# Kernel tuning notes

Measured on AMD Instinct MI355X. Metric: run time of the kernel, lower is better.

Reference implementation:

```python
import jax, jax.numpy as jnp
import numpy as np

STRIDES = (8, 16, 32, 64, 128)
NUM_CLASSES = 80
TOPK = 1000
CONF_THRESH = 0.05
NMS_THRESH = 0.6
IMG_H = IMG_W = 2048
CLASS_OFFSET = 100000.0  # > any box coordinate, makes different-class boxes disjoint


def _level_decode(cls, reg, ctn, scale, stride):
    # cls: [1,C,H,W], reg: [1,4,H,W], ctn: [1,1,H,W]
    C, H, W = cls.shape[1], cls.shape[2], cls.shape[3]
    cls = jnp.transpose(cls[0], (1, 2, 0)).reshape(-1, C)       # [HW, C]
    reg = jnp.transpose(reg[0], (1, 2, 0)).reshape(-1, 4)       # [HW, 4]
    reg = jax.nn.relu(reg * scale) * stride                      # Scale + relu + stride
    ctn = jnp.transpose(ctn[0], (1, 2, 0)).reshape(-1, 1)       # [HW, 1]
    prob = jnp.sqrt(jax.nn.sigmoid(cls) * jax.nn.sigmoid(ctn))  # [HW, C]
    scores = prob.max(axis=-1)
    labels = prob.argmax(axis=-1)
    ys, xs = jnp.meshgrid(jnp.arange(H), jnp.arange(W), indexing='ij')
    anchors = (jnp.stack([xs, ys], axis=-1).reshape(-1, 2).astype(cls.dtype) + 0.5) * stride
    if scores.shape[0] > TOPK:
        scores, idx = jax.lax.top_k(scores, TOPK)
        labels, reg, anchors = labels[idx], reg[idx], anchors[idx]
    # decode (l,t,r,b) deltas around anchor centers -> (x1,y1,x2,y2)
    boxes = jnp.concatenate([anchors - reg[:, :2], anchors + reg[:, 2:]], axis=-1)
    return scores, labels, boxes


def _nms_keep(boxes, scores, valid, thresh):
    # Sequential greedy NMS, same math as the numpy loop in RTEFCOS.nms.
    order = jnp.argsort(-jnp.where(valid, scores, -jnp.inf))
    b = boxes[order]
    v = valid[order]
    x1, y1, x2, y2 = b[:, 0], b[:, 1], b[:, 2], b[:, 3]
    areas = (x2 - x1) * (y2 - y1)
    n = b.shape[0]
    pos = jnp.arange(n)

    def body(i, keep):
        xx1 = jnp.maximum(x1[i], x1)
        yy1 = jnp.maximum(y1[i], y1)
        xx2 = jnp.minimum(x2[i], x2)
        yy2 = jnp.minimum(y2[i], y2)
        inter = jnp.maximum(1e-10, xx2 - xx1) * jnp.maximum(1e-10, yy2 - yy1)
        ovr = inter / (areas[i] + areas - inter + 1e-14)
        suppress = (ovr > thresh) & (pos > i) & keep[i]
        return keep & (~suppress)

    keep_sorted = jax.lax.fori_loop(0, n, body, v)
    return jnp.zeros(n, dtype=bool).at[order].set(keep_sorted)


def reference(cls0, reg0, ctn0, cls1, reg1, ctn1, cls2, reg2, ctn2,
              cls3, reg3, ctn3, cls4, reg4, ctn4, scales):
    levels = [(cls0, reg0, ctn0), (cls1, reg1, ctn1), (cls2, reg2, ctn2),
              (cls3, reg3, ctn3), (cls4, reg4, ctn4)]
    all_s, all_l, all_b = [], [], []
    for lv, (c, r, t) in enumerate(levels):
        s, l, b = _level_decode(c, r, t, scales[lv], STRIDES[lv])
        all_s.append(s); all_l.append(l); all_b.append(b)
    scores = jnp.concatenate(all_s)   # [M]
    labels = jnp.concatenate(all_l)   # [M]
    bboxes = jnp.concatenate(all_b)   # [M, 4]
    valid = scores >= CONF_THRESH     # conf filter as mask (static shapes)
    # class-wise NMS via coordinate-offset trick: boxes of different classes
    # never overlap, so one greedy pass == per-class greedy passes.
    boxes_off = bboxes + labels[:, None].astype(bboxes.dtype) * CLASS_OFFSET
    keep = _nms_keep(boxes_off, scores, valid, NMS_THRESH)
    bboxes = bboxes / jnp.array([IMG_W, IMG_H, IMG_W, IMG_H], dtype=bboxes.dtype)
    bboxes = jnp.clip(bboxes, 0.0, 1.0)
    return bboxes, scores, labels, keep


def setup_inputs():
    key = jax.random.key(0)
    ks = jax.random.split(key, len(STRIDES))
    inp = {}
    for lv, stride in enumerate(STRIDES):
        H = IMG_H // stride
        W = IMG_W // stride
        k1, k2, k3 = jax.random.split(ks[lv], 3)
        inp[f"cls{lv}"] = jax.random.normal(k1, (1, NUM_CLASSES, H, W), jnp.float32)
        inp[f"reg{lv}"] = jax.random.uniform(k2, (1, 4, H, W), jnp.float32)
        inp[f"ctn{lv}"] = jax.random.normal(k3, (1, 1, H, W), jnp.float32)
    inp["scales"] = jnp.ones((5,), jnp.float32)
    return inp
```

## Files before the change

### kernel.cpp

```cpp
#include <hip/hip_runtime.h>
#include <math.h>

#define TOTAL_ANCHORS 87296
#define NTOPK 87040
#define NSEL 4256
#define NWORDS 67
#define NPAD   4288
#define MAXROUNDS 4300
#define CANDMAX 8192
#define NBIN 32768
#define NSLAB 8

__device__ __forceinline__ float sigmoidf_(float x) {
    return 1.0f / (1.0f + expf(-x));
}
__device__ __forceinline__ unsigned int f2s(float f) {
    unsigned int u = __float_as_uint(f);
    return u ^ ((u >> 31) ? 0xFFFFFFFFu : 0x80000000u);
}
__device__ __forceinline__ float s2f(unsigned int k) {
    unsigned int u = (k & 0x80000000u) ? (k ^ 0x80000000u) : ~k;
    return __uint_as_float(u);
}
__device__ __forceinline__ void level_of(int g, int& lv, int& base, int& W, int& stride) {
    if (g < 65536)      { lv = 0; base = 0;     W = 256; stride = 8;   }
    else if (g < 81920) { lv = 1; base = 65536; W = 128; stride = 16;  }
    else if (g < 86016) { lv = 2; base = 81920; W = 64;  stride = 32;  }
    else if (g < 87040) { lv = 3; base = 86016; W = 32;  stride = 64;  }
    else                { lv = 4; base = 87040; W = 16;  stride = 128; }
}

struct InPtrs {
    const float* cls[5];
    const float* reg[5];
    const float* ctn[5];
    const float* scales;
};

__global__ __launch_bounds__(256) void cmax_kernel(InPtrs in,
        unsigned long long* __restrict__ cmax2) {
    int a = blockIdx.x * 256 + threadIdx.x;
    int cg = blockIdx.y;
    int lv, base, W, stride;
    level_of(a, lv, base, W, stride);
    (void)stride;
    int p = a - base;
    int HW = W * W;
    const float* cls = in.cls[lv];
    float sctn = sigmoidf_(in.ctn[lv][p]);
    int c0 = cg * 8;
    float v[8];
    #pragma unroll
    for (int k = 0; k < 8; ++k) v[k] = cls[(c0 + k) * HW + p];
    unsigned long long best = 0ull;
    #pragma unroll
    for (int k = 0; k < 8; ++k) {
        float pr = sqrtf(__fmul_rn(sigmoidf_(v[k]), sctn));
        unsigned long long key = ((unsigned long long)f2s(pr) << 32)
                               | (unsigned long long)(255 - (c0 + k));
        best = (key > best) ? key : best;
    }
    cmax2[(size_t)cg * TOTAL_ANCHORS + a] = best;
}

__global__ __launch_bounds__(256) void decode2_kernel(InPtrs in,
        const unsigned long long* __restrict__ cmax2,
        unsigned long long* __restrict__ keys, float* __restrict__ scores,
        int* __restrict__ labels, float4* __restrict__ boxes) {
    int g = blockIdx.x * 256 + threadIdx.x;
    int lv, base, W, stride;
    level_of(g, lv, base, W, stride);
    int p = g - base;
    int HW = W * W;
    int x = p & (W - 1);
    int y = p / W;
    unsigned long long mk = 0ull;
    #pragma unroll
    for (int cg = 0; cg < 10; ++cg) {
        unsigned long long v = cmax2[(size_t)cg * TOTAL_ANCHORS + g];
        mk = (v > mk) ? v : mk;
    }
    float best = s2f((unsigned int)(mk >> 32));
    int lbl = 255 - (int)(mk & 0xFFull);
    float scale = in.scales[lv];
    float fs = (float)stride;
    const float* rg = in.reg[lv];
    float r0 = __fmul_rn(fmaxf(__fmul_rn(rg[0 * HW + p], scale), 0.0f), fs);
    float r1 = __fmul_rn(fmaxf(__fmul_rn(rg[1 * HW + p], scale), 0.0f), fs);
    float r2 = __fmul_rn(fmaxf(__fmul_rn(rg[2 * HW + p], scale), 0.0f), fs);
    float r3 = __fmul_rn(fmaxf(__fmul_rn(rg[3 * HW + p], scale), 0.0f), fs);
    float ax = __fmul_rn(__fadd_rn((float)x, 0.5f), fs);
    float ay = __fmul_rn(__fadd_rn((float)y, 0.5f), fs);
    float4 b;
    b.x = __fsub_rn(ax, r0);
    b.y = __fsub_rn(ay, r1);
    b.z = __fadd_rn(ax, r2);
    b.w = __fadd_rn(ay, r3);
    scores[g] = best;
    labels[g] = lbl;
    boxes[g]  = b;
    keys[g] = (mk & 0xFFFFFFFF00000000ull)
            | (unsigned long long)(unsigned int)(~(unsigned int)p);
}

__global__ __launch_bounds__(1024) void hist_kernel(
        const unsigned long long* __restrict__ keys,
        unsigned int* __restrict__ slab) {
    __shared__ unsigned int h[NBIN / 2];
    const int starts[NSLAB] = {0, 16384, 32768, 49152, 65536, 73728, 81920, 86016};
    const int ends[NSLAB]   = {16384, 32768, 49152, 65536, 73728, 81920, 86016, 87040};
    const int tid = threadIdx.x;
    for (int i = tid; i < NBIN / 2; i += 1024) h[i] = 0u;
    __syncthreads();
    const int s = starts[blockIdx.x], e = ends[blockIdx.x];
    for (int i = s + tid; i < e; i += 1024) {
        unsigned int bin = (unsigned int)(keys[i] >> 48) & 0x7FFFu;
        atomicAdd(&h[bin >> 1], 1u << ((bin & 1u) << 4));
    }
    __syncthreads();
    unsigned int* out = slab + blockIdx.x * (NBIN / 2);
    for (int i = tid; i < NBIN / 2; i += 1024) out[i] = h[i];
}

__global__ __launch_bounds__(1024) void select_kernel(
        const unsigned int* __restrict__ slab, unsigned int* __restrict__ thr,
        unsigned int* __restrict__ cnt) {
    const int lvl = blockIdx.x;
    const int slabS[4] = {0, 4, 6, 7};
    const int slabE[4] = {4, 6, 7, 8};
    const int tid = threadIdx.x;
    if (lvl == 0 && tid < 128) cnt[tid] = 0u;
    __shared__ unsigned int csum[1024];
    unsigned int s = 0;
    for (int sb = slabS[lvl]; sb < slabE[lvl]; ++sb) {
        const unsigned int* A = slab + sb * (NBIN / 2);
        #pragma unroll 4
        for (int w = tid * 16; w < tid * 16 + 16; ++w) {
            unsigned int v = A[w];
            s += (v & 0xFFFFu) + (v >> 16);
        }
    }
    csum[tid] = s;
    __syncthreads();
    for (int off = 1; off < 1024; off <<= 1) {
        unsigned int v = csum[tid] + ((tid + off < 1024) ? csum[tid + off] : 0u);
        __syncthreads();
        csum[tid] = v;
        __syncthreads();
    }
    unsigned int incl = csum[tid];
    unsigned int incl1 = (tid == 1023) ? 0u : csum[tid + 1];
    if (incl >= 1000u && incl1 < 1000u) {
        unsigned int running = incl1;
        for (int b = tid * 32 + 31; b >= tid * 32; --b) {
            unsigned int c = 0;
            for (int sb = slabS[lvl]; sb < slabE[lvl]; ++sb) {
                unsigned int v = slab[sb * (NBIN / 2) + (b >> 1)];
                c += (v >> ((b & 1) << 4)) & 0xFFFFu;
            }
            running += c;
            if (running >= 1000u) { thr[lvl] = (unsigned int)b; break; }
        }
    }
}

__global__ __launch_bounds__(1024) void gather_kernel(
        const unsigned long long* __restrict__ keys,
        const unsigned int* __restrict__ thr,
        unsigned long long* __restrict__ cand, unsigned int* __restrict__ cnt) {
    int g = blockIdx.x * 1024 + threadIdx.x;
    int lvl;
    if (g < 65536)      lvl = 0;
    else if (g < 81920) lvl = 1;
    else if (g < 86016) lvl = 2;
    else                lvl = 3;
    unsigned long long k = keys[g];
    bool pass = (((unsigned int)(k >> 48)) & 0x7FFFu) >= thr[lvl];
    __shared__ unsigned int woff[16];
    __shared__ unsigned int base_;
    const int wave = threadIdx.x >> 6, lane = threadIdx.x & 63;
    unsigned long long m = __ballot(pass);
    if (lane == 0) woff[wave] = (unsigned int)__popcll(m);
    __syncthreads();
    if (threadIdx.x == 0) {
        unsigned int tot = 0;
        #pragma unroll
        for (int w = 0; w < 16; ++w) { unsigned int c = woff[w]; woff[w] = tot; tot += c; }
        base_ = atomicAdd(&cnt[lvl << 5], tot);
    }
    __syncthreads();
    if (pass) {
        unsigned int pos = base_ + woff[wave]
                         + (unsigned int)__popcll(m & ((1ull << lane) - 1ull));
        if (pos < CANDMAX) cand[(lvl << 13) + pos] = k;
    }
}

__global__ __launch_bounds__(1024) void finalsort_kernel(
        const unsigned long long* __restrict__ cand,
        const unsigned int* __restrict__ cnt,
        unsigned long long* __restrict__ sel) {
    const int lvl = blockIdx.x;
    const int tid = threadIdx.x;
    __shared__ unsigned long long sk[CANDMAX];
    int n = (int)cnt[lvl << 5];
    if (n > CANDMAX) n = CANDMAX;
    int P = 1024;
    while (P < n) P <<= 1;
    for (int i = tid; i < P; i += 1024)
        sk[i] = (i < n) ? cand[(lvl << 13) + i] : 0ull;
    __syncthreads();
    for (int kk = 2; kk <= P; kk <<= 1) {
        for (int j = kk >> 1; j > 0; j >>= 1) {
            for (int i = tid; i < P; i += 1024) {
                int ixj = i ^ j;
                if (ixj > i) {
                    unsigned long long a = sk[i], b = sk[ixj];
                    bool sw = ((i & kk) == 0) ? (a < b) : (a > b);
                    if (sw) { sk[i] = b; sk[ixj] = a; }
                }
            }
            __syncthreads();
        }
    }
    if (tid < 1000) sel[lvl * 1000 + tid] = sk[tid];
}

#define PEND_VEC 3216
__global__ __launch_bounds__(256) void fin_kernel(
        const unsigned long long* __restrict__ sel,
        const float* __restrict__ scores, const int* __restrict__ labels,
        const float4* __restrict__ boxes, float* __restrict__ out,
        float4* __restrict__ entbox, float* __restrict__ entarea,
        int* __restrict__ entvalid, unsigned long long* __restrict__ ekeyG,
        float4* __restrict__ pendzero) {
    int pos = blockIdx.x * 256 + threadIdx.x;
    if (pos < PEND_VEC) pendzero[pos] = make_float4(0.f, 0.f, 0.f, 0.f);
    if (pos >= NSEL) return;
    int g;
    if (pos < 4000) {
        int lv = pos / 1000;
        const int offs_[4] = {0, 65536, 81920, 86016};
        unsigned long long key = sel[pos];
        unsigned int p = ~((unsigned int)(key & 0xFFFFFFFFull));
        g = offs_[lv] + (int)p;
    } else {
        g = 87040 + (pos - 4000);
    }
    float sc = scores[g];
    int lb = labels[g];
    float4 bx = boxes[g];
    const float inv = 1.0f / 2048.0f;
    out[pos * 4 + 0] = fminf(fmaxf(__fmul_rn(bx.x, inv), 0.0f), 1.0f);
    out[pos * 4 + 1] = fminf(fmaxf(__fmul_rn(bx.y, inv), 0.0f), 1.0f);
    out[pos * 4 + 2] = fminf(fmaxf(__fmul_rn(bx.z, inv), 0.0f), 1.0f);
    out[pos * 4 + 3] = fminf(fmaxf(__fmul_rn(bx.w, inv), 0.0f), 1.0f);
    out[17024 + pos] = sc;
    out[21280 + pos] = (float)lb;
    out[25536 + pos] = 0.0f;
    float off = __fmul_rn((float)lb, 100000.0f);
    float4 eb;
    eb.x = __fadd_rn(bx.x, off); eb.y = __fadd_rn(bx.y, off);
    eb.z = __fadd_rn(bx.z, off); eb.w = __fadd_rn(bx.w, off);
    entbox[pos] = eb;
    entarea[pos] = __fmul_rn(__fsub_rn(eb.z, eb.x), __fsub_rn(eb.w, eb.y));
    int valid = (sc >= 0.05f) ? 1 : 0;
    entvalid[pos] = valid;
    float effs = valid ? sc : -INFINITY;
    ekeyG[pos] = ((unsigned long long)f2s(effs) << 32) | (unsigned int)(~(unsigned int)pos);
}

__device__ __forceinline__ int count_greater(const unsigned long long* A, int n,
                                             unsigned long long x) {
    int lo = 0, hi = n;
    while (lo < hi) { int m = (lo + hi) >> 1; if (A[m] > x) lo = m + 1; else hi = m; }
    return lo;
}
__global__ __launch_bounds__(1024) void rank_kernel(
        const unsigned long long* __restrict__ ekeyG,
        const float4* __restrict__ entbox, const float* __restrict__ entarea,
        const int* __restrict__ entvalid,
        int* __restrict__ order, float4* __restrict__ sbox,
        float* __restrict__ sarea, int* __restrict__ svalid) {
    __shared__ unsigned long long eL[4000];
    __shared__ unsigned long long sk4[256];
    const int tid = threadIdx.x;
    for (int i = tid; i < 4000; i += 1024) eL[i] = ekeyG[i];
    if (tid < 256) sk4[tid] = ekeyG[4000 + tid];
    __syncthreads();
    for (int kk = 2; kk <= 256; kk <<= 1) {
        for (int j = kk >> 1; j > 0; j >>= 1) {
            if (tid < 256) {
                int ixj = tid ^ j;
                if (ixj > tid) {
                    unsigned long long a = sk4[tid], b = sk4[ixj];
                    bool sw = ((tid & kk) == 0) ? (a < b) : (a > b);
                    if (sw) { sk4[tid] = b; sk4[ixj] = a; }
                }
            }
            __syncthreads();
        }
    }
    int pos = blockIdx.x * 1024 + tid;
    if (pos < NSEL) {
        unsigned long long x = (pos < 4000) ? eL[pos] : ekeyG[pos];
        int rank = count_greater(eL,        1000, x)
                 + count_greater(eL + 1000, 1000, x)
                 + count_greater(eL + 2000, 1000, x)
                 + count_greater(eL + 3000, 1000, x)
                 + count_greater(sk4,        256, x);
        order[rank]  = pos;
        sbox[rank]   = entbox[pos];
        sarea[rank]  = entarea[pos];
        svalid[rank] = entvalid[pos];
    }
}

__global__ __launch_bounds__(64) void mask_kernel(
        const float4* __restrict__ sbox, const float* __restrict__ sarea,
        const int* __restrict__ svalid,
        unsigned long long* __restrict__ maskC,
        unsigned long long* __restrict__ pend0G,
        unsigned int* __restrict__ pend1G) {
    int colTile = blockIdx.x, rowTile = blockIdx.y;
    if (colTile > rowTile) return;
    __shared__ float4 cb[64];
    __shared__ float ca[64];
    int tid = threadIdx.x;
    int col0 = colTile * 64;
    int c = col0 + tid;
    int vcol = 0;
    if (c < NSEL) { cb[tid] = sbox[c]; ca[tid] = sarea[c]; vcol = svalid[c]; }
    else { cb[tid] = make_float4(0.f, 0.f, 0.f, 0.f); ca[tid] = 0.f; }
    unsigned long long unkw = __ballot(vcol != 0);
    __syncthreads();
    int i = rowTile * 64 + tid;
    unsigned long long bits = 0ull;
    if (i < NSEL) {
        float4 b = sbox[i];
        float ar = sarea[i];
        for (int j = 0; j < 64; ++j) {
            float xx1 = fmaxf(b.x, cb[j].x);
            float yy1 = fmaxf(b.y, cb[j].y);
            float xx2 = fminf(b.z, cb[j].z);
            float yy2 = fminf(b.w, cb[j].w);
            float w = fmaxf(1e-10f, __fsub_rn(xx2, xx1));
            float h = fmaxf(1e-10f, __fsub_rn(yy2, yy1));
            float inter = __fmul_rn(w, h);
            float denom = __fadd_rn(__fsub_rn(__fadd_rn(ar, ca[j]), inter), 1e-14f);
            float ovr = __fdiv_rn(inter, denom);
            if (ovr > 0.6f) bits |= (1ull << j);
        }
    }
    maskC[(size_t)colTile * NPAD + i] = bits;
    if (colTile < rowTile && i < NSEL && (bits & unkw)) {
        if (colTile < 64) atomicOr(&pend0G[i], 1ull << colTile);
        else              atomicOr(&pend1G[i], 1u << (colTile - 64));
    }
}

__global__ __launch_bounds__(1024) void sweep_kernel(
        const unsigned long long* __restrict__ maskC,
        const unsigned long long* __restrict__ pend0G,
        const unsigned int* __restrict__ pend1G,
        const int* __restrict__ order, const int* __restrict__ svalid,
        float* __restrict__ out_keep) {
    const int tid = threadIdx.x;
    const int lane = tid & 63;
    const int wave = tid >> 6;
    __shared__ unsigned long long keptL[NWORDS], unkL[NWORDS];
    __shared__ unsigned long long nk[NWORDS], nkC[NWORDS], ndC[NWORDS];
    __shared__ unsigned long long cm0s;
    __shared__ unsigned int cm1s;
    __shared__ int anych;
    __shared__ int wflag[16];

    unsigned long long md[5], pend0[5];
    unsigned int pendH[5];
    #pragma unroll
    for (int k = 0; k < 5; ++k) {
        int b = wave + 16 * k;
        unsigned long long w = 0ull;
        md[k] = 0ull; pend0[k] = 0ull; pendH[k] = 0u;
        if (b < NWORDS) {
            int c = b * 64 + lane;
            int v = (c < NSEL) ? svalid[c] : 0;
            w = __ballot(v != 0);
            md[k]    = maskC[(size_t)b * NPAD + c];
            pend0[k] = pend0G[c];
            pendH[k] = pend1G[c];
            if (lane == 0) { unkL[b] = w; keptL[b] = 0ull; nk[b] = 0ull; }
        }
    }
    if (tid == 0) { cm0s = 0ull; cm1s = 0u; }
    __syncthreads();

    for (int round = 0; round < MAXROUNDS; ++round) {
        unsigned long long cm0 = cm0s;
        unsigned int cm1 = cm1s;
        #pragma unroll
        for (int k = 0; k < 5; ++k) {
            int b = wave + 16 * k;
            bool kp = false, dec = false;
            if (b < NWORDS) {
                int c = b * 64 + lane;
                unsigned long long uw = unkL[b];
                if ((uw >> lane) & 1ull) {
                    bool rem = false;
                    unsigned long long todo = pend0[k] & cm0;
                    while (todo) {
                        int w = __ffsll((long long)todo) - 1;
                        todo &= todo - 1ull;
                        unsigned long long m = maskC[(size_t)w * NPAD + c];
                        if (m & nk[w]) { rem = true; break; }
                        if ((m & unkL[w]) == 0ull) pend0[k] &= ~(1ull << w);
                    }
                    if (!rem) {
                        unsigned int todoH = pendH[k] & cm1;
                        while (todoH) {
                            int bit = __ffs(todoH) - 1;
                            todoH &= todoH - 1u;
                            int w = 64 + bit;
                            unsigned long long m = maskC[(size_t)w * NPAD + c];
                            if (m & nk[w]) { rem = true; break; }
                            if ((m & unkL[w]) == 0ull) pendH[k] &= ~(1u << bit);
                        }
                    }
                    unsigned long long below = (1ull << lane) - 1ull;
                    if (!rem && (md[k] & keptL[b] & below)) rem = true;
                    if (!rem && pend0[k] == 0ull && pendH[k] == 0u
                             && (md[k] & uw & below) == 0ull) kp = true;
                    dec = rem || kp;
                }
            }
            unsigned long long kb = __ballot(kp);
            unsigned long long db = __ballot(dec);
            if (b < NWORDS && lane == 0) { nkC[b] = kb; ndC[b] = db; }
        }
        __syncthreads();
        int any = 0;
        #pragma unroll
        for (int k = 0; k < 5; ++k) {
            int b = wave + 16 * k;
            if (b >= NWORDS) continue;
            unsigned long long db = ndC[b];
            if (lane == 0) {
                keptL[b] |= nkC[b];
                unkL[b]  &= ~db;
                nk[b]     = nkC[b];
            }
            any |= (db != 0ull) ? 1 : 0;
        }
        if (lane == 0) wflag[wave] = any;
        __syncthreads();
        if (tid == 0) {
            unsigned long long c0 = 0ull; unsigned int c1 = 0u; int a = 0;
            for (int w = 0; w < 64; ++w) if (ndC[w]) c0 |= (1ull << w);
            for (int w = 64; w < NWORDS; ++w) if (ndC[w]) c1 |= (1u << (w - 64));
            #pragma unroll
            for (int w = 0; w < 16; ++w) a |= wflag[w];
            cm0s = c0; cm1s = c1; anych = a;
        }
        __syncthreads();
        if (!anych) break;
    }

    #pragma unroll
    for (int k = 0; k < 5; ++k) {
        int b = wave + 16 * k;
        if (b >= NWORDS) continue;
        int c = b * 64 + lane;
        if (c < NSEL && ((keptL[b] >> lane) & 1ull)) out_keep[order[c]] = 1.0f;
    }
}

constexpr size_t OFF_KEYS    = 0;
constexpr size_t OFF_SCORES  = OFF_KEYS    + 698368;
constexpr size_t OFF_LABELS  = OFF_SCORES  + 349184;
constexpr size_t OFF_BOXES   = OFF_LABELS  + 349184;
constexpr size_t OFF_SEL     = OFF_BOXES   + 1396736;
constexpr size_t OFF_ORDER   = OFF_SEL     + 32000;
constexpr size_t OFF_SBOX    = OFF_ORDER   + 17024;
constexpr size_t OFF_SAREA   = OFF_SBOX    + 68096;
constexpr size_t OFF_SVALID  = OFF_SAREA   + 17024;
constexpr size_t OFF_MASK    = OFF_SVALID  + 17024;
constexpr size_t OFF_CMAX2   = OFF_MASK    + (size_t)NWORDS * NPAD * 8;
constexpr size_t OFF_CNT     = OFF_CMAX2   + 10u * 698368u;
constexpr size_t OFF_PEND0   = OFF_CNT     + 512;
constexpr size_t OFF_PEND1   = OFF_PEND0   + (size_t)NPAD * 8;
constexpr size_t OFF_THR     = OFF_PEND1   + (size_t)NPAD * 4;
constexpr size_t OFF_SLAB    = OFF_THR     + 64;
constexpr size_t OFF_CAND    = OFF_SLAB    + (size_t)NSLAB * 16384u * 4u;
constexpr size_t OFF_EKEY    = OFF_CAND    + 4u * CANDMAX * 8u;
constexpr size_t OFF_ENTBOX  = OFF_EKEY    + 34048;
constexpr size_t OFF_ENTAREA = OFF_ENTBOX  + 68096;
constexpr size_t OFF_ENTVAL  = OFF_ENTAREA + 17024;

extern "C" void kernel_launch(void* const* d_in, const int* in_sizes, int n_in,
                              void* d_out, int out_size, void* d_ws, size_t ws_size,
                              hipStream_t stream) {
    (void)in_sizes; (void)n_in; (void)out_size; (void)ws_size;
    InPtrs P;
    for (int lv = 0; lv < 5; ++lv) {
        P.cls[lv] = (const float*)d_in[3 * lv + 0];
        P.reg[lv] = (const float*)d_in[3 * lv + 1];
        P.ctn[lv] = (const float*)d_in[3 * lv + 2];
    }
    P.scales = (const float*)d_in[15];

    char* ws = (char*)d_ws;
    unsigned long long* keys   = (unsigned long long*)(ws + OFF_KEYS);
    float*              scores = (float*)             (ws + OFF_SCORES);
    int*                labels = (int*)               (ws + OFF_LABELS);
    float4*             boxes  = (float4*)            (ws + OFF_BOXES);
    unsigned long long* sel    = (unsigned long long*)(ws + OFF_SEL);
    int*                order  = (int*)               (ws + OFF_ORDER);
    float4*             sbox   = (float4*)            (ws + OFF_SBOX);
    float*              sarea  = (float*)             (ws + OFF_SAREA);
    int*                svalid = (int*)               (ws + OFF_SVALID);
    unsigned long long* maskb  = (unsigned long long*)(ws + OFF_MASK);
    unsigned long long* cmax2  = (unsigned long long*)(ws + OFF_CMAX2);
    unsigned int*       cnt    = (unsigned int*)      (ws + OFF_CNT);
    unsigned long long* pend0  = (unsigned long long*)(ws + OFF_PEND0);
    unsigned int*       pend1  = (unsigned int*)      (ws + OFF_PEND1);
    unsigned int*       thr    = (unsigned int*)      (ws + OFF_THR);
    unsigned int*       slab   = (unsigned int*)      (ws + OFF_SLAB);
    unsigned long long* cand   = (unsigned long long*)(ws + OFF_CAND);
    unsigned long long* ekeyG  = (unsigned long long*)(ws + OFF_EKEY);
    float4*             entbox = (float4*)            (ws + OFF_ENTBOX);
    float*              entarea= (float*)             (ws + OFF_ENTAREA);
    int*                entval = (int*)               (ws + OFF_ENTVAL);
    float* out = (float*)d_out;

    cmax_kernel<<<dim3(341, 10), 256, 0, stream>>>(P, cmax2);
    decode2_kernel<<<341, 256, 0, stream>>>(P, cmax2, keys, scores, labels, boxes);
    hist_kernel<<<NSLAB, 1024, 0, stream>>>(keys, slab);
    select_kernel<<<4, 1024, 0, stream>>>(slab, thr, cnt);
    gather_kernel<<<85, 1024, 0, stream>>>(keys, thr, cand, cnt);
    finalsort_kernel<<<4, 1024, 0, stream>>>(cand, cnt, sel);
    fin_kernel<<<(NSEL + 255) / 256, 256, 0, stream>>>(sel, scores, labels, boxes, out,
                                                       entbox, entarea, entval, ekeyG,
                                                       (float4*)(ws + OFF_PEND0));
    rank_kernel<<<(NSEL + 1023) / 1024, 1024, 0, stream>>>(ekeyG, entbox, entarea, entval,
                                                           order, sbox, sarea, svalid);
    mask_kernel<<<dim3(NWORDS, NWORDS), 64, 0, stream>>>(sbox, sarea, svalid,
                                                         maskb, pend0, pend1);
    sweep_kernel<<<1, 1024, 0, stream>>>(maskb, pend0, pend1, order, svalid, out + 25536);
}
```

Measured before the change: 120.8 us.

## Vectorize decode kernels, fuse fin into rank, batch mask rows per block

The cmax and decode kernels now handle four anchors per thread with float4 and 128-bit loads and stores. The fin kernel is merged into the rank kernel, so each block rebuilds the sort keys in shared memory and writes the outputs and sorted boxes directly, which removes one launch and the intermediate global buffers. Zeroing of the pending buffers moves into the gather kernel. The mask kernel processes four row tiles per 256-thread block so each column tile is loaded once for all four, at the cost of every finrank block recomputing all keys.

```diff
diff --git a/kernel.cpp b/kernel.cpp
--- a/kernel.cpp
+++ b/kernel.cpp
@@ -10,6 +10,7 @@
 #define CANDMAX 8192
 #define NBIN 32768
 #define NSLAB 8
+#define PEND_VEC 3216
 
 __device__ __forceinline__ float sigmoidf_(float x) {
     return 1.0f / (1.0f + expf(-x));
@@ -21,6 +22,9 @@
 __device__ __forceinline__ float s2f(unsigned int k) {
     unsigned int u = (k & 0x80000000u) ? (k ^ 0x80000000u) : ~k;
     return __uint_as_float(u);
+}
+__device__ __forceinline__ float f4e(const float4& v, int j) {
+    return (j == 0) ? v.x : ((j == 1) ? v.y : ((j == 2) ? v.z : v.w));
 }
 __device__ __forceinline__ void level_of(int g, int& lv, int& base, int& W, int& stride) {
     if (g < 65536)      { lv = 0; base = 0;     W = 256; stride = 8;   }
@@ -39,68 +43,97 @@
 
 __global__ __launch_bounds__(256) void cmax_kernel(InPtrs in,
         unsigned long long* __restrict__ cmax2) {
-    int a = blockIdx.x * 256 + threadIdx.x;
+    int t = blockIdx.x * 256 + threadIdx.x;
+    int a0 = t * 4;
+    if (a0 >= TOTAL_ANCHORS) return;
     int cg = blockIdx.y;
     int lv, base, W, stride;
-    level_of(a, lv, base, W, stride);
+    level_of(a0, lv, base, W, stride);
     (void)stride;
-    int p = a - base;
+    int p0 = a0 - base;
     int HW = W * W;
     const float* cls = in.cls[lv];
-    float sctn = sigmoidf_(in.ctn[lv][p]);
+    float4 ct = *(const float4*)&in.ctn[lv][p0];
+    float sct0 = sigmoidf_(ct.x), sct1 = sigmoidf_(ct.y);
+    float sct2 = sigmoidf_(ct.z), sct3 = sigmoidf_(ct.w);
     int c0 = cg * 8;
-    float v[8];
-    #pragma unroll
-    for (int k = 0; k < 8; ++k) v[k] = cls[(c0 + k) * HW + p];
-    unsigned long long best = 0ull;
+    unsigned long long b0 = 0ull, b1 = 0ull, b2 = 0ull, b3 = 0ull;
     #pragma unroll
     for (int k = 0; k < 8; ++k) {
-        float pr = sqrtf(__fmul_rn(sigmoidf_(v[k]), sctn));
-        unsigned long long key = ((unsigned long long)f2s(pr) << 32)
-                               | (unsigned long long)(255 - (c0 + k));
-        best = (key > best) ? key : best;
-    }
-    cmax2[(size_t)cg * TOTAL_ANCHORS + a] = best;
+        float4 v = *(const float4*)&cls[(c0 + k) * HW + p0];
+        unsigned long long lbl = (unsigned long long)(255 - (c0 + k));
+        unsigned long long k0 = ((unsigned long long)f2s(sqrtf(__fmul_rn(sigmoidf_(v.x), sct0))) << 32) | lbl;
+        unsigned long long k1 = ((unsigned long long)f2s(sqrtf(__fmul_rn(sigmoidf_(v.y), sct1))) << 32) | lbl;
+        unsigned long long k2 = ((unsigned long long)f2s(sqrtf(__fmul_rn(sigmoidf_(v.z), sct2))) << 32) | lbl;
+        unsigned long long k3 = ((unsigned long long)f2s(sqrtf(__fmul_rn(sigmoidf_(v.w), sct3))) << 32) | lbl;
+        b0 = (k0 > b0) ? k0 : b0;
+        b1 = (k1 > b1) ? k1 : b1;
+        b2 = (k2 > b2) ? k2 : b2;
+        b3 = (k3 > b3) ? k3 : b3;
+    }
+    unsigned long long* dst = cmax2 + (size_t)cg * TOTAL_ANCHORS + a0;
+    dst[0] = b0; dst[1] = b1; dst[2] = b2; dst[3] = b3;
 }
 
 __global__ __launch_bounds__(256) void decode2_kernel(InPtrs in,
         const unsigned long long* __restrict__ cmax2,
         unsigned long long* __restrict__ keys, float* __restrict__ scores,
         int* __restrict__ labels, float4* __restrict__ boxes) {
-    int g = blockIdx.x * 256 + threadIdx.x;
+    int t = blockIdx.x * 256 + threadIdx.x;
+    int g0 = t * 4;
+    if (g0 >= TOTAL_ANCHORS) return;
     int lv, base, W, stride;
-    level_of(g, lv, base, W, stride);
-    int p = g - base;
+    level_of(g0, lv, base, W, stride);
+    int p0 = g0 - base;
     int HW = W * W;
-    int x = p & (W - 1);
-    int y = p / W;
-    unsigned long long mk = 0ull;
+    unsigned long long mk0 = 0ull, mk1 = 0ull, mk2 = 0ull, mk3 = 0ull;
     #pragma unroll
     for (int cg = 0; cg < 10; ++cg) {
-        unsigned long long v = cmax2[(size_t)cg * TOTAL_ANCHORS + g];
-        mk = (v > mk) ? v : mk;
-    }
-    float best = s2f((unsigned int)(mk >> 32));
-    int lbl = 255 - (int)(mk & 0xFFull);
+        const ulonglong2* s2 = (const ulonglong2*)(cmax2 + (size_t)cg * TOTAL_ANCHORS + g0);
+        ulonglong2 va = s2[0], vb = s2[1];
+        mk0 = (va.x > mk0) ? va.x : mk0;
+        mk1 = (va.y > mk1) ? va.y : mk1;
+        mk2 = (vb.x > mk2) ? vb.x : mk2;
+        mk3 = (vb.y > mk3) ? vb.y : mk3;
+    }
+    unsigned long long mk[4] = {mk0, mk1, mk2, mk3};
     float scale = in.scales[lv];
     float fs = (float)stride;
     const float* rg = in.reg[lv];
-    float r0 = __fmul_rn(fmaxf(__fmul_rn(rg[0 * HW + p], scale), 0.0f), fs);
-    float r1 = __fmul_rn(fmaxf(__fmul_rn(rg[1 * HW + p], scale), 0.0f), fs);
-    float r2 = __fmul_rn(fmaxf(__fmul_rn(rg[2 * HW + p], scale), 0.0f), fs);
-    float r3 = __fmul_rn(fmaxf(__fmul_rn(rg[3 * HW + p], scale), 0.0f), fs);
-    float ax = __fmul_rn(__fadd_rn((float)x, 0.5f), fs);
-    float ay = __fmul_rn(__fadd_rn((float)y, 0.5f), fs);
-    float4 b;
-    b.x = __fsub_rn(ax, r0);
-    b.y = __fsub_rn(ay, r1);
-    b.z = __fadd_rn(ax, r2);
-    b.w = __fadd_rn(ay, r3);
-    scores[g] = best;
-    labels[g] = lbl;
-    boxes[g]  = b;
-    keys[g] = (mk & 0xFFFFFFFF00000000ull)
-            | (unsigned long long)(unsigned int)(~(unsigned int)p);
+    float4 rq0 = *(const float4*)&rg[0 * HW + p0];
+    float4 rq1 = *(const float4*)&rg[1 * HW + p0];
+    float4 rq2 = *(const float4*)&rg[2 * HW + p0];
+    float4 rq3 = *(const float4*)&rg[3 * HW + p0];
+    float4 sc4;
+    int4 lb4;
+    #pragma unroll
+    for (int j = 0; j < 4; ++j) {
+        int p = p0 + j;
+        int x = p & (W - 1);
+        int y = p / W;
+        float best = s2f((unsigned int)(mk[j] >> 32));
+        int lbl = 255 - (int)(mk[j] & 0xFFull);
+        float r0 = __fmul_rn(fmaxf(__fmul_rn(f4e(rq0, j), scale), 0.0f), fs);
+        float r1 = __fmul_rn(fmaxf(__fmul_rn(f4e(rq1, j), scale), 0.0f), fs);
+        float r2 = __fmul_rn(fmaxf(__fmul_rn(f4e(rq2, j), scale), 0.0f), fs);
+        float r3 = __fmul_rn(fmaxf(__fmul_rn(f4e(rq3, j), scale), 0.0f), fs);
+        float ax = __fmul_rn(__fadd_rn((float)x, 0.5f), fs);
+        float ay = __fmul_rn(__fadd_rn((float)y, 0.5f), fs);
+        float4 b;
+        b.x = __fsub_rn(ax, r0);
+        b.y = __fsub_rn(ay, r1);
+        b.z = __fadd_rn(ax, r2);
+        b.w = __fadd_rn(ay, r3);
+        boxes[g0 + j] = b;
+        keys[g0 + j] = (mk[j] & 0xFFFFFFFF00000000ull)
+                     | (unsigned long long)(unsigned int)(~(unsigned int)(p));
+        if (j == 0) { sc4.x = best; lb4.x = lbl; }
+        else if (j == 1) { sc4.y = best; lb4.y = lbl; }
+        else if (j == 2) { sc4.z = best; lb4.z = lbl; }
+        else { sc4.w = best; lb4.w = lbl; }
+    }
+    *(float4*)&scores[g0] = sc4;
+    *(int4*)&labels[g0] = lb4;
 }
 
 __global__ __launch_bounds__(1024) void hist_kernel(
@@ -167,7 +200,12 @@
 __global__ __launch_bounds__(1024) void gather_kernel(
         const unsigned long long* __restrict__ keys,
         const unsigned int* __restrict__ thr,
-        unsigned long long* __restrict__ cand, unsigned int* __restrict__ cnt) {
+        unsigned long long* __restrict__ cand, unsigned int* __restrict__ cnt,
+        float4* __restrict__ pendzero) {
+    if (blockIdx.x < 4) {
+        int z = blockIdx.x * 1024 + threadIdx.x;
+        if (z < PEND_VEC) pendzero[z] = make_float4(0.f, 0.f, 0.f, 0.f);
+    }
     int g = blockIdx.x * 1024 + threadIdx.x;
     int lvl;
     if (g < 65536)      lvl = 0;
@@ -226,67 +264,46 @@
     if (tid < 1000) sel[lvl * 1000 + tid] = sk[tid];
 }
 
-#define PEND_VEC 3216
-__global__ __launch_bounds__(256) void fin_kernel(
-        const unsigned long long* __restrict__ sel,
-        const float* __restrict__ scores, const int* __restrict__ labels,
-        const float4* __restrict__ boxes, float* __restrict__ out,
-        float4* __restrict__ entbox, float* __restrict__ entarea,
-        int* __restrict__ entvalid, unsigned long long* __restrict__ ekeyG,
-        float4* __restrict__ pendzero) {
-    int pos = blockIdx.x * 256 + threadIdx.x;
-    if (pos < PEND_VEC) pendzero[pos] = make_float4(0.f, 0.f, 0.f, 0.f);
-    if (pos >= NSEL) return;
-    int g;
-    if (pos < 4000) {
-        int lv = pos / 1000;
-        const int offs_[4] = {0, 65536, 81920, 86016};
-        unsigned long long key = sel[pos];
-        unsigned int p = ~((unsigned int)(key & 0xFFFFFFFFull));
-        g = offs_[lv] + (int)p;
-    } else {
-        g = 87040 + (pos - 4000);
-    }
-    float sc = scores[g];
-    int lb = labels[g];
-    float4 bx = boxes[g];
-    const float inv = 1.0f / 2048.0f;
-    out[pos * 4 + 0] = fminf(fmaxf(__fmul_rn(bx.x, inv), 0.0f), 1.0f);
-    out[pos * 4 + 1] = fminf(fmaxf(__fmul_rn(bx.y, inv), 0.0f), 1.0f);
-    out[pos * 4 + 2] = fminf(fmaxf(__fmul_rn(bx.z, inv), 0.0f), 1.0f);
-    out[pos * 4 + 3] = fminf(fmaxf(__fmul_rn(bx.w, inv), 0.0f), 1.0f);
-    out[17024 + pos] = sc;
-    out[21280 + pos] = (float)lb;
-    out[25536 + pos] = 0.0f;
-    float off = __fmul_rn((float)lb, 100000.0f);
-    float4 eb;
-    eb.x = __fadd_rn(bx.x, off); eb.y = __fadd_rn(bx.y, off);
-    eb.z = __fadd_rn(bx.z, off); eb.w = __fadd_rn(bx.w, off);
-    entbox[pos] = eb;
-    entarea[pos] = __fmul_rn(__fsub_rn(eb.z, eb.x), __fsub_rn(eb.w, eb.y));
-    int valid = (sc >= 0.05f) ? 1 : 0;
-    entvalid[pos] = valid;
-    float effs = valid ? sc : -INFINITY;
-    ekeyG[pos] = ((unsigned long long)f2s(effs) << 32) | (unsigned int)(~(unsigned int)pos);
-}
-
 __device__ __forceinline__ int count_greater(const unsigned long long* A, int n,
                                              unsigned long long x) {
     int lo = 0, hi = n;
     while (lo < hi) { int m = (lo + hi) >> 1; if (A[m] > x) lo = m + 1; else hi = m; }
     return lo;
 }
-__global__ __launch_bounds__(1024) void rank_kernel(
-        const unsigned long long* __restrict__ ekeyG,
-        const float4* __restrict__ entbox, const float* __restrict__ entarea,
-        const int* __restrict__ entvalid,
+__global__ __launch_bounds__(1024) void finrank_kernel(
+        const unsigned long long* __restrict__ sel,
+        const float* __restrict__ scores, const int* __restrict__ labels,
+        const float4* __restrict__ boxes, float* __restrict__ out,
         int* __restrict__ order, float4* __restrict__ sbox,
         float* __restrict__ sarea, int* __restrict__ svalid) {
-    __shared__ unsigned long long eL[4000];
+    __shared__ unsigned long long eL[NSEL];
     __shared__ unsigned long long sk4[256];
     const int tid = threadIdx.x;
-    for (int i = tid; i < 4000; i += 1024) eL[i] = ekeyG[i];
-    if (tid < 256) sk4[tid] = ekeyG[4000 + tid];
+    const int blk = blockIdx.x;
+    int gown = 0; float scown = 0.f; int vown = 0;
+    #pragma unroll
+    for (int k = 0; k < 5; ++k) {
+        int pos = tid + k * 1024;
+        if (pos < NSEL) {
+            int g;
+            if (pos < 4000) {
+                int lvp = pos / 1000;
+                const int offs_[4] = {0, 65536, 81920, 86016};
+                unsigned long long key = sel[pos];
+                unsigned int p = ~((unsigned int)(key & 0xFFFFFFFFull));
+                g = offs_[lvp] + (int)p;
+            } else {
+                g = 87040 + (pos - 4000);
+            }
+            float sc = scores[g];
+            int valid = (sc >= 0.05f) ? 1 : 0;
+            float effs = valid ? sc : -INFINITY;
+            eL[pos] = ((unsigned long long)f2s(effs) << 32) | (unsigned int)(~(unsigned int)pos);
+            if (k == blk) { gown = g; scown = sc; vown = valid; }
+        }
+    }
+    __syncthreads();
+    if (tid < 256) sk4[tid] = eL[4000 + tid];
     __syncthreads();
     for (int kk = 2; kk <= 256; kk <<= 1) {
         for (int j = kk >> 1; j > 0; j >>= 1) {
@@ -301,40 +318,62 @@
             __syncthreads();
         }
     }
-    int pos = blockIdx.x * 1024 + tid;
+    int pos = blk * 1024 + tid;
     if (pos < NSEL) {
-        unsigned long long x = (pos < 4000) ? eL[pos] : ekeyG[pos];
+        int lb = labels[gown];
+        float4 bx = boxes[gown];
+        const float inv = 1.0f / 2048.0f;
+        float4 o4;
+        o4.x = fminf(fmaxf(__fmul_rn(bx.x, inv), 0.0f), 1.0f);
+        o4.y = fminf(fmaxf(__fmul_rn(bx.y, inv), 0.0f), 1.0f);
+        o4.z = fminf(fmaxf(__fmul_rn(bx.z, inv), 0.0f), 1.0f);
+        o4.w = fminf(fmaxf(__fmul_rn(bx.w, inv), 0.0f), 1.0f);
+        *(float4*)&out[pos * 4] = o4;
+        out[17024 + pos] = scown;
+        out[21280 + pos] = (float)lb;
+        out[25536 + pos] = 0.0f;
+        float off = __fmul_rn((float)lb, 100000.0f);
+        float4 eb;
+        eb.x = __fadd_rn(bx.x, off); eb.y = __fadd_rn(bx.y, off);
+        eb.z = __fadd_rn(bx.z, off); eb.w = __fadd_rn(bx.w, off);
+        float area = __fmul_rn(__fsub_rn(eb.z, eb.x), __fsub_rn(eb.w, eb.y));
+        unsigned long long x = eL[pos];
         int rank = count_greater(eL,        1000, x)
                  + count_greater(eL + 1000, 1000, x)
                  + count_greater(eL + 2000, 1000, x)
                  + count_greater(eL + 3000, 1000, x)
                  + count_greater(sk4,        256, x);
         order[rank]  = pos;
-        sbox[rank]   = entbox[pos];
-        sarea[rank]  = entarea[pos];
-        svalid[rank] = entvalid[pos];
-    }
-}
-
-__global__ __launch_bounds__(64) void mask_kernel(
+        sbox[rank]   = eb;
+        sarea[rank]  = area;
+        svalid[rank] = vown;
+    }
+}
+
+__global__ __launch_bounds__(256) void mask_kernel(
         const float4* __restrict__ sbox, const float* __restrict__ sarea,
         const int* __restrict__ svalid,
         unsigned long long* __restrict__ maskC,
         unsigned long long* __restrict__ pend0G,
         unsigned int* __restrict__ pend1G) {
-    int colTile = blockIdx.x, rowTile = blockIdx.y;
-    if (colTile > rowTile) return;
+    const int colTile = blockIdx.x;
+    const int tid = threadIdx.x;
+    const int lane = tid & 63;
+    const int rowTile = blockIdx.y * 4 + (tid >> 6);
     __shared__ float4 cb[64];
     __shared__ float ca[64];
-    int tid = threadIdx.x;
     int col0 = colTile * 64;
-    int c = col0 + tid;
-    int vcol = 0;
-    if (c < NSEL) { cb[tid] = sbox[c]; ca[tid] = sarea[c]; vcol = svalid[c]; }
-    else { cb[tid] = make_float4(0.f, 0.f, 0.f, 0.f); ca[tid] = 0.f; }
+    if (tid < 64) {
+        int c = col0 + tid;
+        if (c < NSEL) { cb[tid] = sbox[c]; ca[tid] = sarea[c]; }
+        else { cb[tid] = make_float4(0.f, 0.f, 0.f, 0.f); ca[tid] = 0.f; }
+    }
+    __syncthreads();
+    if (rowTile >= NWORDS || colTile > rowTile) return;
+    int cc = col0 + lane;
+    int vcol = (cc < NSEL) ? svalid[cc] : 0;
     unsigned long long unkw = __ballot(vcol != 0);
-    __syncthreads();
-    int i = rowTile * 64 + tid;
+    int i = rowTile * 64 + lane;
     unsigned long long bits = 0ull;
     if (i < NSEL) {
         float4 b = sbox[i];
@@ -491,10 +530,6 @@
 constexpr size_t OFF_THR     = OFF_PEND1   + (size_t)NPAD * 4;
 constexpr size_t OFF_SLAB    = OFF_THR     + 64;
 constexpr size_t OFF_CAND    = OFF_SLAB    + (size_t)NSLAB * 16384u * 4u;
-constexpr size_t OFF_EKEY    = OFF_CAND    + 4u * CANDMAX * 8u;
-constexpr size_t OFF_ENTBOX  = OFF_EKEY    + 34048;
-constexpr size_t OFF_ENTAREA = OFF_ENTBOX  + 68096;
-constexpr size_t OFF_ENTVAL  = OFF_ENTAREA + 17024;
 
 extern "C" void kernel_launch(void* const* d_in, const int* in_sizes, int n_in,
                               void* d_out, int out_size, void* d_ws, size_t ws_size,
@@ -526,24 +561,19 @@
     unsigned int*       thr    = (unsigned int*)      (ws + OFF_THR);
     unsigned int*       slab   = (unsigned int*)      (ws + OFF_SLAB);
     unsigned long long* cand   = (unsigned long long*)(ws + OFF_CAND);
-    unsigned long long* ekeyG  = (unsigned long long*)(ws + OFF_EKEY);
-    float4*             entbox = (float4*)            (ws + OFF_ENTBOX);
-    float*              entarea= (float*)             (ws + OFF_ENTAREA);
-    int*                entval = (int*)               (ws + OFF_ENTVAL);
     float* out = (float*)d_out;
 
-    cmax_kernel<<<dim3(341, 10), 256, 0, stream>>>(P, cmax2);
-    decode2_kernel<<<341, 256, 0, stream>>>(P, cmax2, keys, scores, labels, boxes);
+    const int quarter_blocks = (TOTAL_ANCHORS / 4 + 255) / 256;
+    cmax_kernel<<<dim3(quarter_blocks, 10), 256, 0, stream>>>(P, cmax2);
+    decode2_kernel<<<quarter_blocks, 256, 0, stream>>>(P, cmax2, keys, scores, labels, boxes);
     hist_kernel<<<NSLAB, 1024, 0, stream>>>(keys, slab);
     select_kernel<<<4, 1024, 0, stream>>>(slab, thr, cnt);
-    gather_kernel<<<85, 1024, 0, stream>>>(keys, thr, cand, cnt);
+    gather_kernel<<<85, 1024, 0, stream>>>(keys, thr, cand, cnt,
+                                           (float4*)(ws + OFF_PEND0));
     finalsort_kernel<<<4, 1024, 0, stream>>>(cand, cnt, sel);
-    fin_kernel<<<(NSEL + 255) / 256, 256, 0, stream>>>(sel, scores, labels, boxes, out,
-                                                       entbox, entarea, entval, ekeyG,
-                                                       (float4*)(ws + OFF_PEND0));
-    rank_kernel<<<(NSEL + 1023) / 1024, 1024, 0, stream>>>(ekeyG, entbox, entarea, entval,
-                                                           order, sbox, sarea, svalid);
-    mask_kernel<<<dim3(NWORDS, NWORDS), 64, 0, stream>>>(sbox, sarea, svalid,
-                                                         maskb, pend0, pend1);
+    finrank_kernel<<<5, 1024, 0, stream>>>(sel, scores, labels, boxes, out,
+                                           order, sbox, sarea, svalid);
+    mask_kernel<<<dim3(NWORDS, (NWORDS + 3) / 4), 256, 0, stream>>>(sbox, sarea, svalid,
+                                                                    maskb, pend0, pend1);
     sweep_kernel<<<1, 1024, 0, stream>>>(maskb, pend0, pend1, order, svalid, out + 25536);
 }
```

After: 122.6 us. About the same (+1.5%).
